# Kernel optimization log

Hardware: AMD Instinct MI355X
Metric: run time of the kernel (lower is better)

Reference implementation:

```python
import jax, jax.numpy as jnp
import numpy as np

LN_EPS = 1e-5


def setup_inputs() -> dict:
    key = jax.random.key(0)
    k_x, k_w = jax.random.split(key)
    B, T, F, M = 128, 512, 512, 512
    x = jax.random.normal(k_x, (B, T, F), dtype=jnp.float32)
    gamma = jnp.ones((T,), dtype=jnp.float32)
    beta = jnp.zeros((T,), dtype=jnp.float32)
    W = jax.random.normal(k_w, (M, T), dtype=jnp.float32) * 0.02  # Linear(T -> M) weight
    b = jnp.zeros((M,), dtype=jnp.float32)
    return {"x": x, "gamma": gamma, "beta": beta, "W": W, "b": b}


def reference(x, gamma, beta, W, b):
    # x: [B, T, F]. LayerNorm over the time axis T per (batch, feature) row,
    # matching norm(x.permute(0,2,1).reshape(-1, T)).
    mean = jnp.mean(x, axis=1, keepdims=True)                 # [B,1,F]
    var = jnp.mean((x - mean) ** 2, axis=1, keepdims=True)     # [B,1,F]
    xn = (x - mean) * jax.lax.rsqrt(var + LN_EPS)
    xn = xn * gamma[None, :, None] + beta[None, :, None]       # [B,T,F]
    # time_mlp: Linear along T (applied to [B,F,T] rows), output [B,F,M]
    # expressed directly in [B,T,F] layout -> [B,M,F]
    y = jnp.einsum('btf,mt->bmf', xn, W) + b[None, :, None]
    y = jax.nn.gelu(y, approximate=False)                      # torch nn.GELU is exact
    # dropout_prob = 0.0 -> identity; residual (M == T)
    return y + x
```

## Files before the change

### kernel.cpp

```cpp
#include <hip/hip_runtime.h>
#include <hip/hip_bf16.h>
#include <cstdint>


#define B_ 128
#define T_ 512
#define F_ 512
#define M_ 512
#define FT 32
#define XN_STRIDE 520

typedef __attribute__((ext_vector_type(8))) short bf16x8;
typedef __attribute__((ext_vector_type(4))) float f32x4;

static __device__ __forceinline__ unsigned short f2bf(float f) {
    unsigned int u = __float_as_uint(f);
    unsigned int r = u + 0x7FFFu + ((u >> 16) & 1u);
    return (unsigned short)(r >> 16);
}

__global__ void wconv_kernel(const float* __restrict__ W, unsigned short* __restrict__ Wq) {
    int idx  = blockIdx.x * 256 + threadIdx.x;
    int lane = idx & 63;
    int mg   = (idx >> 6) & 31;
    int kc   = idx >> 11;
    int m = mg * 16 + (lane & 15);
    int k = kc * 32 + (lane >> 4) * 8;
    const float* src = W + (size_t)m * 512 + k;
    float4 v0 = *(const float4*)(src);
    float4 v1 = *(const float4*)(src + 4);
    uint4 o;
    o.x = (unsigned int)f2bf(v0.x) | ((unsigned int)f2bf(v0.y) << 16);
    o.y = (unsigned int)f2bf(v0.z) | ((unsigned int)f2bf(v0.w) << 16);
    o.z = (unsigned int)f2bf(v1.x) | ((unsigned int)f2bf(v1.y) << 16);
    o.w = (unsigned int)f2bf(v1.z) | ((unsigned int)f2bf(v1.w) << 16);
    *(uint4*)(Wq + (size_t)idx * 8) = o;
}

__global__ __launch_bounds__(512, 4) void timemix_main(
    const float* __restrict__ x, const float* __restrict__ gamma,
    const float* __restrict__ beta, const unsigned short* __restrict__ Wq,
    const float* __restrict__ bias, float* __restrict__ out)
{
    __shared__ __align__(16) unsigned char smem[37632];
    unsigned char* xnS = smem;
    float* gS    = (float*)(smem + 33280);
    float* bS    = (float*)(smem + 35328);
    float* meanS = (float*)(smem + 37376);
    float* rstdS = (float*)(smem + 37504);
    __shared__ float red_sum[16 * 32];
    __shared__ float red_sq[16 * 32];

    const int tid   = threadIdx.x;
    const int w     = tid >> 6;
    const int lane  = tid & 63;
    const int batch = blockIdx.y;
    const int f0    = blockIdx.x * FT;

    gS[tid] = gamma[tid];
    bS[tid] = beta[tid];

    const int f  = lane & 31;
    const int tg = w * 2 + (lane >> 5);
    float xv[32];
    {
        const float* xb = x + ((size_t)batch * T_ + (size_t)tg * 32) * F_ + f0 + f;
        float s = 0.f, q = 0.f;
        #pragma unroll
        for (int i = 0; i < 32; ++i) {
            float v = xb[(size_t)i * F_];
            xv[i] = v; s += v; q += v * v;
        }
        red_sum[tg * 32 + f] = s;
        red_sq [tg * 32 + f] = q;
    }
    __syncthreads();

    if (tid < 32) {
        float s = 0.f, q = 0.f;
        #pragma unroll
        for (int g = 0; g < 16; ++g) { s += red_sum[g * 32 + tid]; q += red_sq[g * 32 + tid]; }
        float mean = s * (1.0f / 512.0f);
        float var  = q * (1.0f / 512.0f) - mean * mean;
        meanS[tid] = mean;
        rstdS[tid] = rsqrtf(var + 1e-5f);
    }
    __syncthreads();

    {
        const float mean = meanS[f];
        const float rstd = rstdS[f];
        #pragma unroll
        for (int c = 0; c < 4; ++c) {
            const int t0 = tg * 32 + c * 8;
            unsigned int pr[4];
            #pragma unroll
            for (int h = 0; h < 4; ++h) {
                float a0 = rstd * gS[t0 + 2 * h];
                float v0 = xv[c * 8 + 2 * h] * a0 + (bS[t0 + 2 * h] - mean * a0);
                float a1 = rstd * gS[t0 + 2 * h + 1];
                float v1 = xv[c * 8 + 2 * h + 1] * a1 + (bS[t0 + 2 * h + 1] - mean * a1);
                pr[h] = (unsigned int)f2bf(v0) | ((unsigned int)f2bf(v1) << 16);
            }
            uint4 pk; pk.x = pr[0]; pk.y = pr[1]; pk.z = pr[2]; pk.w = pr[3];
            *(uint4*)(xnS + (size_t)f * (XN_STRIDE * 2) + t0 * 2) = pk;
        }
    }
    __syncthreads();

    const int lr = lane & 15;
    const int q4 = lane >> 4;
    const unsigned short* wbase = Wq + ((size_t)(w * 4) * 64 + lane) * 8;

    f32x4 acc[4][2];
    #pragma unroll
    for (int mi = 0; mi < 4; ++mi)
        #pragma unroll
        for (int fi = 0; fi < 2; ++fi)
            acc[mi][fi] = (f32x4){0.f, 0.f, 0.f, 0.f};

    bf16x8 aA[4], aB[4];
    #pragma unroll
    for (int mi = 0; mi < 4; ++mi)
        aA[mi] = *(const bf16x8*)(wbase + (size_t)mi * 512);

    for (int kc = 0; kc < 16; kc += 2) {
        #pragma unroll
        for (int mi = 0; mi < 4; ++mi)
            aB[mi] = *(const bf16x8*)(wbase + (size_t)(kc + 1) * 16384 + (size_t)mi * 512);
        {
            bf16x8 b0 = *(const bf16x8*)(xnS + (size_t)lr * (XN_STRIDE * 2) + kc * 64 + q4 * 16);
            bf16x8 b1 = *(const bf16x8*)(xnS + (size_t)(16 + lr) * (XN_STRIDE * 2) + kc * 64 + q4 * 16);
            #pragma unroll
            for (int mi = 0; mi < 4; ++mi) {
                acc[mi][0] = __builtin_amdgcn_mfma_f32_16x16x32_bf16(aA[mi], b0, acc[mi][0], 0, 0, 0);
                acc[mi][1] = __builtin_amdgcn_mfma_f32_16x16x32_bf16(aA[mi], b1, acc[mi][1], 0, 0, 0);
            }
        }
        if (kc + 2 < 16) {
            #pragma unroll
            for (int mi = 0; mi < 4; ++mi)
                aA[mi] = *(const bf16x8*)(wbase + (size_t)(kc + 2) * 16384 + (size_t)mi * 512);
        }
        {
            bf16x8 b0 = *(const bf16x8*)(xnS + (size_t)lr * (XN_STRIDE * 2) + (kc + 1) * 64 + q4 * 16);
            bf16x8 b1 = *(const bf16x8*)(xnS + (size_t)(16 + lr) * (XN_STRIDE * 2) + (kc + 1) * 64 + q4 * 16);
            #pragma unroll
            for (int mi = 0; mi < 4; ++mi) {
                acc[mi][0] = __builtin_amdgcn_mfma_f32_16x16x32_bf16(aB[mi], b0, acc[mi][0], 0, 0, 0);
                acc[mi][1] = __builtin_amdgcn_mfma_f32_16x16x32_bf16(aB[mi], b1, acc[mi][1], 0, 0, 0);
            }
        }
    }

    #pragma unroll
    for (int mi = 0; mi < 4; ++mi) {
        const int mbase = w * 64 + mi * 16 + q4 * 4;
        #pragma unroll
        for (int r = 0; r < 4; ++r) {
            const int m = mbase + r;
            const float bv = bias[m];
            #pragma unroll
            for (int fi = 0; fi < 2; ++fi) {
                float y = acc[mi][fi][r] + bv;
                float gl = 0.5f * y * (1.0f + erff(y * 0.70710678118654752f));
                size_t o = ((size_t)(batch * 512 + m)) * 512 + (size_t)(f0 + fi * 16 + lr);
                out[o] = gl + x[o];
            }
        }
    }
}

extern "C" void kernel_launch(void* const* d_in, const int* in_sizes, int n_in,
                              void* d_out, int out_size, void* d_ws, size_t ws_size,
                              hipStream_t stream) {
    const float* x     = (const float*)d_in[0];
    const float* gamma = (const float*)d_in[1];
    const float* beta  = (const float*)d_in[2];
    const float* W     = (const float*)d_in[3];
    const float* bias  = (const float*)d_in[4];
    float* out = (float*)d_out;
    unsigned short* Wq = (unsigned short*)d_ws;

    wconv_kernel<<<dim3(128), 256, 0, stream>>>(W, Wq);
    dim3 grid(F_ / FT, B_);
    timemix_main<<<grid, 512, 0, stream>>>(x, gamma, beta, Wq, bias, out);
}
```

Baseline: 303.8 us.

## Split LayerNorm into separate kernel and use larger-tile register-blocked GEMM

Splits the fused kernel in two. A LayerNorm kernel writes bf16-normalized activations to workspace, laid out in MFMA fragment order. A separate GEMM kernel then computes 256x128 output tiles per block, with each wave holding 4x8 MFMA accumulators and loading both operands directly from global memory. The larger tiles reuse W across many more features and remove the LDS staging. The cost is an extra round trip of the bf16 activation tensor through HBM, plus high register pressure. The old fused kernel is kept as a fallback when the workspace is too small.

```diff
diff --git a/kernel.cpp b/kernel.cpp
--- a/kernel.cpp
+++ b/kernel.cpp
@@ -7,8 +7,6 @@
 #define T_ 512
 #define F_ 512
 #define M_ 512
-#define FT 32
-#define XN_STRIDE 520
 
 typedef __attribute__((ext_vector_type(8))) short bf16x8;
 typedef __attribute__((ext_vector_type(4))) float f32x4;
@@ -37,7 +35,153 @@
     *(uint4*)(Wq + (size_t)idx * 8) = o;
 }
 
-__global__ __launch_bounds__(512, 4) void timemix_main(
+__global__ __launch_bounds__(512) void ln_kernel(
+    const float* __restrict__ x, const float* __restrict__ gamma,
+    const float* __restrict__ beta, unsigned short* __restrict__ xq)
+{
+    __shared__ float red_sum[512];
+    __shared__ float red_sq[512];
+    __shared__ float gS[512];
+    __shared__ float bS[512];
+    __shared__ float meanS[32];
+    __shared__ float rstdS[32];
+
+    const int tid   = threadIdx.x;
+    const int w     = tid >> 6;
+    const int lane  = tid & 63;
+    const int batch = blockIdx.y;
+    const int f0    = blockIdx.x * 32;
+
+    gS[tid] = gamma[tid];
+    bS[tid] = beta[tid];
+
+    const int f  = lane & 31;
+    const int tg = w * 2 + (lane >> 5);
+    float xv[32];
+    {
+        const float* xb = x + ((size_t)batch * T_ + (size_t)tg * 32) * F_ + f0 + f;
+        float s = 0.f, q = 0.f;
+        #pragma unroll
+        for (int i = 0; i < 32; ++i) {
+            float v = xb[(size_t)i * F_];
+            xv[i] = v; s += v; q += v * v;
+        }
+        red_sum[tg * 32 + f] = s;
+        red_sq [tg * 32 + f] = q;
+    }
+    __syncthreads();
+
+    if (tid < 32) {
+        float s = 0.f, q = 0.f;
+        #pragma unroll
+        for (int g = 0; g < 16; ++g) { s += red_sum[g * 32 + tid]; q += red_sq[g * 32 + tid]; }
+        float mean = s * (1.0f / 512.0f);
+        float var  = q * (1.0f / 512.0f) - mean * mean;
+        meanS[tid] = mean;
+        rstdS[tid] = rsqrtf(var + 1e-5f);
+    }
+    __syncthreads();
+
+    {
+        const float mean = meanS[f];
+        const float rstd = rstdS[f];
+        const size_t cbase = ((size_t)(batch * 16 + tg) * 32 + (f0 >> 4) + (f >> 4)) * 64 + (f & 15);
+        #pragma unroll
+        for (int c = 0; c < 4; ++c) {
+            const int t0 = tg * 32 + c * 8;
+            unsigned int pr[4];
+            #pragma unroll
+            for (int h = 0; h < 4; ++h) {
+                float a0 = rstd * gS[t0 + 2 * h];
+                float v0 = xv[c * 8 + 2 * h] * a0 + (bS[t0 + 2 * h] - mean * a0);
+                float a1 = rstd * gS[t0 + 2 * h + 1];
+                float v1 = xv[c * 8 + 2 * h + 1] * a1 + (bS[t0 + 2 * h + 1] - mean * a1);
+                pr[h] = (unsigned int)f2bf(v0) | ((unsigned int)f2bf(v1) << 16);
+            }
+            uint4 pk; pk.x = pr[0]; pk.y = pr[1]; pk.z = pr[2]; pk.w = pr[3];
+            *(uint4*)(xq + (cbase + (size_t)c * 16) * 8) = pk;
+        }
+    }
+}
+
+__global__ __launch_bounds__(256, 2) void gemm_kernel(
+    const float* __restrict__ x, const unsigned short* __restrict__ Wq,
+    const unsigned short* __restrict__ xq, const float* __restrict__ bias,
+    float* __restrict__ out)
+{
+    const int tid  = threadIdx.x;
+    const int w    = tid >> 6;
+    const int lane = tid & 63;
+    const int mb   = blockIdx.x & 1;
+    const int ft   = blockIdx.x >> 1;
+    const int b    = blockIdx.y;
+    const int lr   = lane & 15;
+    const int q4   = lane >> 4;
+
+    const unsigned short* wbase = Wq + ((size_t)(mb * 16 + w * 4) * 64 + lane) * 8;
+    const unsigned short* xbase = xq + (((size_t)(b * 16) * 32) + ft * 8) * 512 + (size_t)lane * 8;
+
+    f32x4 acc[4][8];
+    #pragma unroll
+    for (int mi = 0; mi < 4; ++mi)
+        #pragma unroll
+        for (int fi = 0; fi < 8; ++fi)
+            acc[mi][fi] = (f32x4){0.f, 0.f, 0.f, 0.f};
+
+    bf16x8 A0[4], A1[4], B0[8], B1[8];
+    #pragma unroll
+    for (int mi = 0; mi < 4; ++mi) A0[mi] = *(const bf16x8*)(wbase + (size_t)mi * 512);
+    #pragma unroll
+    for (int fi = 0; fi < 8; ++fi) B0[fi] = *(const bf16x8*)(xbase + (size_t)fi * 512);
+
+    for (int kc = 0; kc < 16; kc += 2) {
+        #pragma unroll
+        for (int mi = 0; mi < 4; ++mi)
+            A1[mi] = *(const bf16x8*)(wbase + (size_t)((kc + 1) * 32 + mi) * 512);
+        #pragma unroll
+        for (int fi = 0; fi < 8; ++fi)
+            B1[fi] = *(const bf16x8*)(xbase + (size_t)((kc + 1) * 32 + fi) * 512);
+        #pragma unroll
+        for (int mi = 0; mi < 4; ++mi)
+            #pragma unroll
+            for (int fi = 0; fi < 8; ++fi)
+                acc[mi][fi] = __builtin_amdgcn_mfma_f32_16x16x32_bf16(A0[mi], B0[fi], acc[mi][fi], 0, 0, 0);
+        if (kc + 2 < 16) {
+            #pragma unroll
+            for (int mi = 0; mi < 4; ++mi)
+                A0[mi] = *(const bf16x8*)(wbase + (size_t)((kc + 2) * 32 + mi) * 512);
+            #pragma unroll
+            for (int fi = 0; fi < 8; ++fi)
+                B0[fi] = *(const bf16x8*)(xbase + (size_t)((kc + 2) * 32 + fi) * 512);
+        }
+        #pragma unroll
+        for (int mi = 0; mi < 4; ++mi)
+            #pragma unroll
+            for (int fi = 0; fi < 8; ++fi)
+                acc[mi][fi] = __builtin_amdgcn_mfma_f32_16x16x32_bf16(A1[mi], B1[fi], acc[mi][fi], 0, 0, 0);
+    }
+
+    #pragma unroll
+    for (int mi = 0; mi < 4; ++mi) {
+        const int mbase = mb * 256 + w * 64 + mi * 16 + q4 * 4;
+        #pragma unroll
+        for (int r = 0; r < 4; ++r) {
+            const int m = mbase + r;
+            const float bv = bias[m];
+            const size_t orow = ((size_t)(b * 512 + m)) * 512 + (size_t)(ft * 128 + lr);
+            #pragma unroll
+            for (int fi = 0; fi < 8; ++fi) {
+                float y = acc[mi][fi][r] + bv;
+                float gl = 0.5f * y * (1.0f + erff(y * 0.70710678118654752f));
+                size_t o = orow + (size_t)(fi * 16);
+                out[o] = gl + x[o];
+            }
+        }
+    }
+}
+
+#define XN_STRIDE 520
+__global__ __launch_bounds__(512, 4) void timemix_fused(
     const float* __restrict__ x, const float* __restrict__ gamma,
     const float* __restrict__ beta, const unsigned short* __restrict__ Wq,
     const float* __restrict__ bias, float* __restrict__ out)
@@ -48,48 +192,32 @@
     float* bS    = (float*)(smem + 35328);
     float* meanS = (float*)(smem + 37376);
     float* rstdS = (float*)(smem + 37504);
-    __shared__ float red_sum[16 * 32];
-    __shared__ float red_sq[16 * 32];
-
-    const int tid   = threadIdx.x;
-    const int w     = tid >> 6;
-    const int lane  = tid & 63;
-    const int batch = blockIdx.y;
-    const int f0    = blockIdx.x * FT;
-
-    gS[tid] = gamma[tid];
-    bS[tid] = beta[tid];
-
-    const int f  = lane & 31;
-    const int tg = w * 2 + (lane >> 5);
+    __shared__ float red_sum[512];
+    __shared__ float red_sq[512];
+
+    const int tid = threadIdx.x, w = tid >> 6, lane = tid & 63;
+    const int batch = blockIdx.y, f0 = blockIdx.x * 32;
+    gS[tid] = gamma[tid]; bS[tid] = beta[tid];
+    const int f = lane & 31, tg = w * 2 + (lane >> 5);
     float xv[32];
     {
         const float* xb = x + ((size_t)batch * T_ + (size_t)tg * 32) * F_ + f0 + f;
         float s = 0.f, q = 0.f;
         #pragma unroll
-        for (int i = 0; i < 32; ++i) {
-            float v = xb[(size_t)i * F_];
-            xv[i] = v; s += v; q += v * v;
-        }
-        red_sum[tg * 32 + f] = s;
-        red_sq [tg * 32 + f] = q;
-    }
-    __syncthreads();
-
+        for (int i = 0; i < 32; ++i) { float v = xb[(size_t)i * F_]; xv[i] = v; s += v; q += v * v; }
+        red_sum[tg * 32 + f] = s; red_sq[tg * 32 + f] = q;
+    }
+    __syncthreads();
     if (tid < 32) {
         float s = 0.f, q = 0.f;
         #pragma unroll
         for (int g = 0; g < 16; ++g) { s += red_sum[g * 32 + tid]; q += red_sq[g * 32 + tid]; }
-        float mean = s * (1.0f / 512.0f);
-        float var  = q * (1.0f / 512.0f) - mean * mean;
-        meanS[tid] = mean;
-        rstdS[tid] = rsqrtf(var + 1e-5f);
-    }
-    __syncthreads();
-
+        float mean = s * (1.0f / 512.0f), var = q * (1.0f / 512.0f) - mean * mean;
+        meanS[tid] = mean; rstdS[tid] = rsqrtf(var + 1e-5f);
+    }
+    __syncthreads();
     {
-        const float mean = meanS[f];
-        const float rstd = rstdS[f];
+        const float mean = meanS[f], rstd = rstdS[f];
         #pragma unroll
         for (int c = 0; c < 4; ++c) {
             const int t0 = tg * 32 + c * 8;
@@ -107,23 +235,16 @@
         }
     }
     __syncthreads();
-
-    const int lr = lane & 15;
-    const int q4 = lane >> 4;
+    const int lr = lane & 15, q4 = lane >> 4;
     const unsigned short* wbase = Wq + ((size_t)(w * 4) * 64 + lane) * 8;
-
     f32x4 acc[4][2];
     #pragma unroll
     for (int mi = 0; mi < 4; ++mi)
         #pragma unroll
-        for (int fi = 0; fi < 2; ++fi)
-            acc[mi][fi] = (f32x4){0.f, 0.f, 0.f, 0.f};
-
+        for (int fi = 0; fi < 2; ++fi) acc[mi][fi] = (f32x4){0.f, 0.f, 0.f, 0.f};
     bf16x8 aA[4], aB[4];
     #pragma unroll
-    for (int mi = 0; mi < 4; ++mi)
-        aA[mi] = *(const bf16x8*)(wbase + (size_t)mi * 512);
-
+    for (int mi = 0; mi < 4; ++mi) aA[mi] = *(const bf16x8*)(wbase + (size_t)mi * 512);
     for (int kc = 0; kc < 16; kc += 2) {
         #pragma unroll
         for (int mi = 0; mi < 4; ++mi)
@@ -152,7 +273,6 @@
             }
         }
     }
-
     #pragma unroll
     for (int mi = 0; mi < 4; ++mi) {
         const int mbase = w * 64 + mi * 16 + q4 * 4;
@@ -180,9 +300,15 @@
     const float* W     = (const float*)d_in[3];
     const float* bias  = (const float*)d_in[4];
     float* out = (float*)d_out;
+
     unsigned short* Wq = (unsigned short*)d_ws;
+    unsigned short* xq = (unsigned short*)((char*)d_ws + 524288);
 
     wconv_kernel<<<dim3(128), 256, 0, stream>>>(W, Wq);
-    dim3 grid(F_ / FT, B_);
-    timemix_main<<<grid, 512, 0, stream>>>(x, gamma, beta, Wq, bias, out);
-}
+    if (ws_size >= (size_t)524288 + (size_t)B_ * 16 * 32 * 64 * 16) {
+        ln_kernel<<<dim3(16, B_), 512, 0, stream>>>(x, gamma, beta, xq);
+        gemm_kernel<<<dim3(8, B_), 256, 0, stream>>>(x, Wq, xq, bias, out);
+    } else {
+        timemix_fused<<<dim3(16, B_), 512, 0, stream>>>(x, gamma, beta, Wq, bias, out);
+    }
+}
```

Result: slower. 377.1 us (+24.1%).
